# Kernel tuning notes

Measured on AMD Instinct MI355X. Metric: run time of the kernel, lower is better.

Reference implementation:

```python
import jax, jax.numpy as jnp
import numpy as np

P_SCALE = 5.0
Q_SCALE = 0.3
EPS = 1e-06
NORM_EPS = 1e-12


def stack3x3_same(img):
    """im2col for 3x3 kernel, 'same' zero padding, stride 1.
    img: (B,H,W,C) -> (B,H,W,9,C), tap order row-major (dy,dx) in {-1,0,1}^2,
    matching the TF stack3x3 ordering with clip=0, pad=1."""
    B, H, W, C = img.shape
    padded = jnp.pad(img, ((0, 0), (1, 1), (1, 1), (0, 0)))
    taps = [padded[:, dy:dy + H, dx:dx + W, :] for dy in range(3) for dx in range(3)]
    return jnp.stack(taps, axis=3)


def setup_inputs() -> dict:
    key = jax.random.key(0)
    k1, k2 = jax.random.split(key)
    B, H, W, C = 32, 64, 64, 64
    n_kernels, ksize = 128, 3
    inputs = jax.random.normal(k1, (B, H, W, C), dtype=jnp.float32)
    # glorot-uniform-ish weight, shape (1, C*k*k, n_kernels)
    fan_in = C * ksize * ksize
    limit = np.sqrt(6.0 / (fan_in + n_kernels)).astype(np.float32)
    w = jax.random.uniform(k2, (1, fan_in, n_kernels), dtype=jnp.float32,
                           minval=-limit, maxval=limit)
    p = jnp.full((n_kernels,), 0.7 * P_SCALE, dtype=jnp.float32)
    q = jnp.full((1,), 1.0 * Q_SCALE, dtype=jnp.float32)
    return {"inputs": inputs, "w": w, "p": p, "q": q}


def reference(inputs, w, p, q):
    B, H, W, C = inputs.shape
    n_kernels = w.shape[-1]
    ksq = w.shape[1] // C  # kernel_size^2 = 9

    # im2col: (B, H*W, C*9), tap-major flatten (matches tf stack axis=3 + reshape)
    x = stack3x3_same(inputs).reshape(B, H * W, ksq * C)

    p_eff = jnp.exp(p / P_SCALE)            # (n_kernels,)
    q_eff = jnp.exp(-q / Q_SCALE)           # (1,)

    # L2 norms (sqrt of clamped square-sum), matching l2_normal
    x_norm = jnp.sqrt(jnp.maximum(jnp.sum(x * x, axis=2, keepdims=True), NORM_EPS)) + q_eff
    w_norm = jnp.sqrt(jnp.maximum(jnp.sum(w * w, axis=1, keepdims=True), NORM_EPS))

    # cosine-similarity matmul: (B, HW, K) x (1, K, N) -> (B, HW, N)
    sim = jnp.einsum('bsk,kn->bsn', x / x_norm, (w / w_norm)[0])

    # sharpened rescaling: sign(x) * (|x| + eps)^p
    out = jnp.sign(sim) * jnp.power(jnp.abs(sim) + EPS, p_eff)
    return out.reshape(B, H, W, n_kernels)
```

## Files before the change

### kernel.cpp

```cpp
#include <hip/hip_runtime.h>
#include <hip/hip_bf16.h>


typedef short bf16x8 __attribute__((ext_vector_type(8)));
typedef float f32x16 __attribute__((ext_vector_type(16)));

__device__ __forceinline__ unsigned short f2bf(float f) {
    union { float f; unsigned int u; } v; v.f = f;
    unsigned int u = v.u;
    unsigned int r = (u + 0x7fffu + ((u >> 16) & 1u)) >> 16;
    return (unsigned short)r;
}

__global__ void prep_w_kernel(const float* __restrict__ w,
                              unsigned short* __restrict__ wn2) {
    const int n = blockIdx.x;
    const int lane = threadIdx.x;
    float vals[9];
    float s = 0.f;
#pragma unroll
    for (int i = 0; i < 9; ++i) {
        float v = w[(i * 64 + lane) * 128 + n];
        vals[i] = v;
        s += v * v;
    }
#pragma unroll
    for (int off = 1; off < 64; off <<= 1) s += __shfl_xor(s, off);
    const float inv = 1.0f / sqrtf(fmaxf(s, 1e-12f));
    const int kc = lane >> 5, koff = lane & 31;
#pragma unroll
    for (int i = 0; i < 9; ++i)
        wn2[((i * 2 + kc) * 128 + n) * 32 + koff] = f2bf(vals[i] * inv);
}

__global__ __launch_bounds__(256, 4) void cossim_main(
    const float* __restrict__ in, const unsigned short* __restrict__ wn,
    const float* __restrict__ p, const float* __restrict__ q,
    float* __restrict__ out) {
    __shared__ unsigned short A[4 * 66 * 72];
    __shared__ float rcsum[256];
    __shared__ float xni[128];
    __shared__ float pfs[128];

    const int tid = (int)threadIdx.x;
    const int l = ((int)blockIdx.x & 7) * 128 + ((int)blockIdx.x >> 3);
    const int b = l >> 5, y0 = (l & 31) * 2;

    if (tid < 128) pfs[tid] = expf(p[tid] * 0.2f);

    {
        const int r = tid >> 6;
        const int col = tid & 63;
        const int row = y0 + r - 1;
        unsigned short* dst = &A[(r * 66 + col + 1) * 72];
        float s = 0.f;
        if ((unsigned)row < 64u) {
            const float4* src = reinterpret_cast<const float4*>(
                in + (size_t)b * 262144 + row * 4096 + col * 64);
#pragma unroll
            for (int it = 0; it < 8; ++it) {
                float4 v0 = src[2 * it];
                float4 v1 = src[2 * it + 1];
                s += v0.x * v0.x + v0.y * v0.y + v0.z * v0.z + v0.w * v0.w;
                s += v1.x * v1.x + v1.y * v1.y + v1.z * v1.z + v1.w * v1.w;
                union { float f; unsigned u; } ux, uy, uz, uw;
                uint4 pk;
                ux.f = v0.x; uy.f = v0.y; uz.f = v0.z; uw.f = v0.w;
                pk.x = __builtin_amdgcn_perm(uy.u + 0x8000u, ux.u + 0x8000u, 0x07060302u);
                pk.y = __builtin_amdgcn_perm(uw.u + 0x8000u, uz.u + 0x8000u, 0x07060302u);
                ux.f = v1.x; uy.f = v1.y; uz.f = v1.z; uw.f = v1.w;
                pk.z = __builtin_amdgcn_perm(uy.u + 0x8000u, ux.u + 0x8000u, 0x07060302u);
                pk.w = __builtin_amdgcn_perm(uw.u + 0x8000u, uz.u + 0x8000u, 0x07060302u);
                *reinterpret_cast<uint4*>(dst + it * 8) = pk;
            }
        } else {
            uint4 z; z.x = z.y = z.z = z.w = 0u;
#pragma unroll
            for (int it = 0; it < 8; ++it)
                *reinterpret_cast<uint4*>(dst + it * 8) = z;
        }
        rcsum[tid] = s;
    }
    if (tid < 64) {
        const int r = tid >> 4, side = (tid >> 3) & 1, ch = (tid & 7) * 8;
        uint4 z; z.x = z.y = z.z = z.w = 0u;
        *reinterpret_cast<uint4*>(&A[(r * 66 + side * 65) * 72 + ch]) = z;
    }
    __syncthreads();

    if (tid < 128) {
        const int ry = tid >> 6, x = tid & 63;
        const float qe = expf(q[0] * (-1.0f / 0.3f));
        float s = 0.f;
#pragma unroll
        for (int dy = 0; dy < 3; ++dy) {
            const float* rs = &rcsum[(ry + dy) * 64];
            if (x > 0) s += rs[x - 1];
            s += rs[x];
            if (x < 63) s += rs[x + 1];
        }
        xni[tid] = 1.0f / (sqrtf(fmaxf(s, 1e-12f)) + qe);
    }
    __syncthreads();

    const int wv = tid >> 6, lane = tid & 63;
    const int ln31 = lane & 31, khi = lane >> 5;
    const int wm = wv >> 1, wnh = wv & 1;
    f32x16 acc00 = {}, acc01 = {}, acc10 = {}, acc11 = {};
    const unsigned short* wB = wn + (wnh * 64 + ln31) * 32 + khi * 8;

    bf16x8 bc00 = *reinterpret_cast<const bf16x8*>(wB);
    bf16x8 bc01 = *reinterpret_cast<const bf16x8*>(wB + 16);
    bf16x8 bc10 = *reinterpret_cast<const bf16x8*>(wB + 1024);
    bf16x8 bc11 = *reinterpret_cast<const bf16x8*>(wB + 1040);

#pragma unroll
    for (int s = 0; s < 18; ++s) {
        bf16x8 bn00, bn01, bn10, bn11;
        if (s + 1 < 18) {
            const unsigned short* wt = wB + (s + 1) * 4096;
            bn00 = *reinterpret_cast<const bf16x8*>(wt);
            bn01 = *reinterpret_cast<const bf16x8*>(wt + 16);
            bn10 = *reinterpret_cast<const bf16x8*>(wt + 1024);
            bn11 = *reinterpret_cast<const bf16x8*>(wt + 1040);
        }
        const int dy = s / 6, dx = (s >> 1) % 3, kc = s & 1;
        const unsigned short* arow =
            &A[((wm + dy) * 66 + ln31 + dx) * 72 + kc * 32 + khi * 8];
        {
            bf16x8 a0 = *reinterpret_cast<const bf16x8*>(arow);
            bf16x8 a1 = *reinterpret_cast<const bf16x8*>(arow + 16);
            acc00 = __builtin_amdgcn_mfma_f32_32x32x16_bf16(a0, bc00, acc00, 0, 0, 0);
            acc01 = __builtin_amdgcn_mfma_f32_32x32x16_bf16(a0, bc10, acc01, 0, 0, 0);
            acc00 = __builtin_amdgcn_mfma_f32_32x32x16_bf16(a1, bc01, acc00, 0, 0, 0);
            acc01 = __builtin_amdgcn_mfma_f32_32x32x16_bf16(a1, bc11, acc01, 0, 0, 0);
        }
        {
            bf16x8 a0 = *reinterpret_cast<const bf16x8*>(arow + 32 * 72);
            bf16x8 a1 = *reinterpret_cast<const bf16x8*>(arow + 32 * 72 + 16);
            acc10 = __builtin_amdgcn_mfma_f32_32x32x16_bf16(a0, bc00, acc10, 0, 0, 0);
            acc11 = __builtin_amdgcn_mfma_f32_32x32x16_bf16(a0, bc10, acc11, 0, 0, 0);
            acc10 = __builtin_amdgcn_mfma_f32_32x32x16_bf16(a1, bc01, acc10, 0, 0, 0);
            acc11 = __builtin_amdgcn_mfma_f32_32x32x16_bf16(a1, bc11, acc11, 0, 0, 0);
        }
        bc00 = bn00; bc01 = bn01; bc10 = bn10; bc11 = bn11;
    }

    float* orow = out + ((size_t)(b * 64 + y0 + wm) * 64) * 128;
#pragma unroll
    for (int tm = 0; tm < 2; ++tm) {
#pragma unroll
        for (int tn = 0; tn < 2; ++tn) {
            const f32x16& av = tm == 0 ? (tn == 0 ? acc00 : acc01)
                                       : (tn == 0 ? acc10 : acc11);
            const int n = wnh * 64 + tn * 32 + ln31;
            const float pn = pfs[n];
#pragma unroll
            for (int r = 0; r < 16; ++r) {
                const int px = tm * 32 + (r & 3) + 8 * (r >> 2) + 4 * khi;
                float sim = av[r] * xni[wm * 64 + px];
                float aa = fabsf(sim) + 1e-6f;
                float rr = exp2f(pn * log2f(aa));
                orow[(size_t)px * 128 + n] = copysignf(rr, sim);
            }
        }
    }
}

extern "C" void kernel_launch(void* const* d_in, const int* in_sizes, int n_in,
                              void* d_out, int out_size, void* d_ws, size_t ws_size,
                              hipStream_t stream) {
    (void)in_sizes; (void)n_in; (void)out_size; (void)ws_size;
    const float* in = (const float*)d_in[0];
    const float* w  = (const float*)d_in[1];
    const float* p  = (const float*)d_in[2];
    const float* q  = (const float*)d_in[3];
    float* out = (float*)d_out;
    unsigned short* wn = (unsigned short*)d_ws;

    prep_w_kernel<<<128, 64, 0, stream>>>(w, wn);
    cossim_main<<<1024, 256, 0, stream>>>(in, wn, p, q, out);
}
```

Before: 44.24 us.

## Double threads per block, split MFMA tiles and staging across eight waves

Moves the main kernel from 256 to 512 threads per block. Each wave now computes one 32x64 output tile (two accumulators) instead of four, and each input pixel row load is split across two threads, with a shuffle combining the partial square-sums. The p exponent is computed per lane in registers instead of staged through shared memory. The aim is more waves in flight to hide global load latency and the epilogue pow cost. In exchange each wave reuses its B fragments across fewer MFMAs, so every wave still loads the full weight stream for its column half, roughly doubling weight-load traffic per block.

```diff
diff --git a/kernel.cpp b/kernel.cpp
--- a/kernel.cpp
+++ b/kernel.cpp
@@ -33,32 +33,29 @@
         wn2[((i * 2 + kc) * 128 + n) * 32 + koff] = f2bf(vals[i] * inv);
 }
 
-__global__ __launch_bounds__(256, 4) void cossim_main(
+__global__ __launch_bounds__(512, 8) void cossim_main(
     const float* __restrict__ in, const unsigned short* __restrict__ wn,
     const float* __restrict__ p, const float* __restrict__ q,
     float* __restrict__ out) {
     __shared__ unsigned short A[4 * 66 * 72];
     __shared__ float rcsum[256];
     __shared__ float xni[128];
-    __shared__ float pfs[128];
 
     const int tid = (int)threadIdx.x;
     const int l = ((int)blockIdx.x & 7) * 128 + ((int)blockIdx.x >> 3);
     const int b = l >> 5, y0 = (l & 31) * 2;
 
-    if (tid < 128) pfs[tid] = expf(p[tid] * 0.2f);
-
     {
-        const int r = tid >> 6;
-        const int col = tid & 63;
+        const int unit = tid >> 1, h = tid & 1;
+        const int r = unit >> 6, col = unit & 63;
         const int row = y0 + r - 1;
-        unsigned short* dst = &A[(r * 66 + col + 1) * 72];
+        unsigned short* dst = &A[(r * 66 + col + 1) * 72 + h * 32];
         float s = 0.f;
         if ((unsigned)row < 64u) {
             const float4* src = reinterpret_cast<const float4*>(
-                in + (size_t)b * 262144 + row * 4096 + col * 64);
+                in + (size_t)b * 262144 + row * 4096 + col * 64 + h * 32);
 #pragma unroll
-            for (int it = 0; it < 8; ++it) {
+            for (int it = 0; it < 4; ++it) {
                 float4 v0 = src[2 * it];
                 float4 v1 = src[2 * it + 1];
                 s += v0.x * v0.x + v0.y * v0.y + v0.z * v0.z + v0.w * v0.w;
@@ -76,10 +73,11 @@
         } else {
             uint4 z; z.x = z.y = z.z = z.w = 0u;
 #pragma unroll
-            for (int it = 0; it < 8; ++it)
+            for (int it = 0; it < 4; ++it)
                 *reinterpret_cast<uint4*>(dst + it * 8) = z;
         }
-        rcsum[tid] = s;
+        s += __shfl_xor(s, 1);
+        if (h == 0) rcsum[unit] = s;
     }
     if (tid < 64) {
         const int r = tid >> 4, side = (tid >> 3) & 1, ch = (tid & 7) * 8;
@@ -105,9 +103,12 @@
 
     const int wv = tid >> 6, lane = tid & 63;
     const int ln31 = lane & 31, khi = lane >> 5;
-    const int wm = wv >> 1, wnh = wv & 1;
-    f32x16 acc00 = {}, acc01 = {}, acc10 = {}, acc11 = {};
-    const unsigned short* wB = wn + (wnh * 64 + ln31) * 32 + khi * 8;
+    const int wm2 = wv >> 1;
+    const int rt = wm2 >> 1;
+    const int xb = (wm2 & 1) * 32;
+    const int wq = wv & 1;
+    f32x16 acc0 = {}, acc1 = {};
+    const unsigned short* wB = wn + (wq * 64 + ln31) * 32 + khi * 8;
 
     bf16x8 bc00 = *reinterpret_cast<const bf16x8*>(wB);
     bf16x8 bc01 = *reinterpret_cast<const bf16x8*>(wB + 16);
@@ -126,43 +127,35 @@
         }
         const int dy = s / 6, dx = (s >> 1) % 3, kc = s & 1;
         const unsigned short* arow =
-            &A[((wm + dy) * 66 + ln31 + dx) * 72 + kc * 32 + khi * 8];
-        {
-            bf16x8 a0 = *reinterpret_cast<const bf16x8*>(arow);
-            bf16x8 a1 = *reinterpret_cast<const bf16x8*>(arow + 16);
-            acc00 = __builtin_amdgcn_mfma_f32_32x32x16_bf16(a0, bc00, acc00, 0, 0, 0);
-            acc01 = __builtin_amdgcn_mfma_f32_32x32x16_bf16(a0, bc10, acc01, 0, 0, 0);
-            acc00 = __builtin_amdgcn_mfma_f32_32x32x16_bf16(a1, bc01, acc00, 0, 0, 0);
-            acc01 = __builtin_amdgcn_mfma_f32_32x32x16_bf16(a1, bc11, acc01, 0, 0, 0);
-        }
-        {
-            bf16x8 a0 = *reinterpret_cast<const bf16x8*>(arow + 32 * 72);
-            bf16x8 a1 = *reinterpret_cast<const bf16x8*>(arow + 32 * 72 + 16);
-            acc10 = __builtin_amdgcn_mfma_f32_32x32x16_bf16(a0, bc00, acc10, 0, 0, 0);
-            acc11 = __builtin_amdgcn_mfma_f32_32x32x16_bf16(a0, bc10, acc11, 0, 0, 0);
-            acc10 = __builtin_amdgcn_mfma_f32_32x32x16_bf16(a1, bc01, acc10, 0, 0, 0);
-            acc11 = __builtin_amdgcn_mfma_f32_32x32x16_bf16(a1, bc11, acc11, 0, 0, 0);
-        }
+            &A[((rt + dy) * 66 + xb + ln31 + dx) * 72 + kc * 32 + khi * 8];
+        bf16x8 a0 = *reinterpret_cast<const bf16x8*>(arow);
+        bf16x8 a1 = *reinterpret_cast<const bf16x8*>(arow + 16);
+        acc0 = __builtin_amdgcn_mfma_f32_32x32x16_bf16(a0, bc00, acc0, 0, 0, 0);
+        acc1 = __builtin_amdgcn_mfma_f32_32x32x16_bf16(a0, bc10, acc1, 0, 0, 0);
+        acc0 = __builtin_amdgcn_mfma_f32_32x32x16_bf16(a1, bc01, acc0, 0, 0, 0);
+        acc1 = __builtin_amdgcn_mfma_f32_32x32x16_bf16(a1, bc11, acc1, 0, 0, 0);
         bc00 = bn00; bc01 = bn01; bc10 = bn10; bc11 = bn11;
     }
 
-    float* orow = out + ((size_t)(b * 64 + y0 + wm) * 64) * 128;
+    const int n0 = wq * 64 + ln31;
+    const float pn0 = expf(p[n0] * 0.2f);
+    const float pn1 = expf(p[n0 + 32] * 0.2f);
+    float* orow = out + ((size_t)(b * 64 + y0 + rt) * 64) * 128;
 #pragma unroll
-    for (int tm = 0; tm < 2; ++tm) {
-#pragma unroll
-        for (int tn = 0; tn < 2; ++tn) {
-            const f32x16& av = tm == 0 ? (tn == 0 ? acc00 : acc01)
-                                       : (tn == 0 ? acc10 : acc11);
-            const int n = wnh * 64 + tn * 32 + ln31;
-            const float pn = pfs[n];
-#pragma unroll
-            for (int r = 0; r < 16; ++r) {
-                const int px = tm * 32 + (r & 3) + 8 * (r >> 2) + 4 * khi;
-                float sim = av[r] * xni[wm * 64 + px];
-                float aa = fabsf(sim) + 1e-6f;
-                float rr = exp2f(pn * log2f(aa));
-                orow[(size_t)px * 128 + n] = copysignf(rr, sim);
-            }
+    for (int r = 0; r < 16; ++r) {
+        const int px = xb + (r & 3) + 8 * (r >> 2) + 4 * khi;
+        const float xn = xni[rt * 64 + px];
+        {
+            float sim = acc0[r] * xn;
+            float aa = fabsf(sim) + 1e-6f;
+            float rr = exp2f(pn0 * log2f(aa));
+            orow[(size_t)px * 128 + n0] = copysignf(rr, sim);
+        }
+        {
+            float sim = acc1[r] * xn;
+            float aa = fabsf(sim) + 1e-6f;
+            float rr = exp2f(pn1 * log2f(aa));
+            orow[(size_t)px * 128 + n0 + 32] = copysignf(rr, sim);
         }
     }
 }
@@ -179,5 +172,5 @@
     unsigned short* wn = (unsigned short*)d_ws;
 
     prep_w_kernel<<<128, 64, 0, stream>>>(w, wn);
-    cossim_main<<<1024, 256, 0, stream>>>(in, wn, p, q, out);
+    cossim_main<<<1024, 512, 0, stream>>>(in, wn, p, q, out);
 }
```

New measurement: 60.25 us. +36.2%, slower.
